# Kernel tuning notes

Hardware: AMD Instinct MI355X
Metric: run time of the kernel (lower is better)

## Reference

```python
import jax, jax.numpy as jnp
import numpy as np

G_K = 16
BN_EPS = 1e-5


def knn_idx(x, k):
    # x: (B, N, C) -> idx: (B, N, k) indices of k nearest neighbors (incl. self)
    sq = jnp.sum(x * x, axis=-1)                       # (B, N)
    d = sq[:, :, None] + sq[:, None, :] - 2.0 * jnp.einsum('bnc,bmc->bnm', x, x)
    _, idx = jax.lax.top_k(-d, k)                      # smallest distances
    return idx


def setup_inputs() -> dict:
    key = jax.random.key(0)
    k1, k2 = jax.random.split(key)
    B, N, C, D = 4, 8192, 3, 64
    x = jax.random.normal(k1, (B, N, C), dtype=jnp.float32)
    W = jax.random.normal(k2, (3 * C, D), dtype=jnp.float32) * 0.1
    b = jnp.zeros((D,), dtype=jnp.float32)
    gamma = jnp.ones((D,), dtype=jnp.float32)
    beta = jnp.zeros((D,), dtype=jnp.float32)
    return {"x": x, "W": W, "b": b, "gamma": gamma, "beta": beta}


def reference(x, W, b, gamma, beta):
    # KNN query (int indices, non-differentiable as in torch)
    idx = knn_idx(x, G_K)                              # (B, N, k)
    # gather-group neighbors: (B, N, k, C)
    x_ne = jax.vmap(lambda xb, ib: xb[ib])(x, idx)
    x_ce = jnp.broadcast_to(x[:, :, None, :], x_ne.shape)
    feat = jnp.concatenate([x_ce, x_ne - x_ce, x_ne], axis=-1)  # (B, N, k, 3C)
    # 1x1 conv == per-(point,neighbor) linear
    h = jnp.einsum('bnkc,cd->bnkd', feat, W) + b       # (B, N, k, D)
    # BatchNorm over (B, N, k) per channel (training-mode batch stats)
    mean = jnp.mean(h, axis=(0, 1, 2))
    var = jnp.var(h, axis=(0, 1, 2))
    h = gamma * (h - mean) * jax.lax.rsqrt(var + BN_EPS) + beta
    h = jax.nn.relu(h)
    # max-pool over neighbors k
    return jnp.max(h, axis=2)                          # (B, N, D)
```

## Files before the change

### kernel.cpp

```cpp
#include <hip/hip_runtime.h>

#define NPTS 8192
#define NB 4
#define KNN 16
#define DCH 64
#define CAP 128
#define WR 8

#define WS_XQ 0
#define WS_XS 524288
#define WS_IB 1048576
#define WS_ST 2097152
#define WS_SS 2097664

__device__ __forceinline__ float vkey(float4 q, float4 c) {
    return __fmaf_rn(q.x, c.x, __fmaf_rn(q.y, c.y, __fmaf_rn(q.z, c.z, c.w)));
}

__global__ __launch_bounds__(256) void k1_prep(const float* __restrict__ x, float4* __restrict__ xq,
                                               float4* __restrict__ xs) {
    int p = blockIdx.x * 256 + threadIdx.x;
    if (p >= NB * NPTS) return;
    float x0 = x[p * 3 + 0], x1 = x[p * 3 + 1], x2 = x[p * 3 + 2];
    float sq = __fmaf_rn(x0, x0, __fmaf_rn(x1, x1, x2 * x2));
    xq[p] = make_float4(x0, x1, x2, sq);
    xs[p] = make_float4(-2.0f * x0, -2.0f * x1, -2.0f * x2, sq);
}

__global__ __launch_bounds__(256, 4) void k2_knn(const float4* __restrict__ xq,
                                                 const float4* __restrict__ xs,
                                                 unsigned short* __restrict__ ibuf) {
    __shared__ float2 buf[4][WR][CAP];
    __shared__ float vmin[4][WR][64];
    const int wave = threadIdx.x >> 6;
    const int lane = threadIdx.x & 63;
    const int b = blockIdx.x >> 8;
    const int blkrow = (blockIdx.x & 255) * (4 * WR);
    const float4* xb = xq + b * NPTS;
    const float4* xc = xs + b * NPTS;
    const int rowbase = blkrow + wave * WR;

    float4 xi[WR];
#pragma unroll
    for (int r = 0; r < WR; ++r) xi[r] = xb[rowbase + r];

    float mn[WR];
#pragma unroll
    for (int r = 0; r < WR; ++r) mn[r] = 3.0e38f;

    {
        const float4* p = xc + lane;
        float4 a0 = p[0], a1 = p[64], a2 = p[128], a3 = p[192];
        for (int c0 = 0; c0 < NPTS - 256; c0 += 256) {
            const float4* pn = p + 256;
            float4 b0 = pn[0], b1 = pn[64], b2 = pn[128], b3 = pn[192];
#pragma unroll
            for (int r = 0; r < WR; ++r) {
                float v0 = vkey(xi[r], a0);
                float v1 = vkey(xi[r], a1);
                float v2 = vkey(xi[r], a2);
                float v3 = vkey(xi[r], a3);
                mn[r] = fminf(mn[r], fminf(v0, v1));
                mn[r] = fminf(mn[r], fminf(v2, v3));
            }
            a0 = b0; a1 = b1; a2 = b2; a3 = b3; p = pn;
        }
#pragma unroll
        for (int r = 0; r < WR; ++r) {
            float v0 = vkey(xi[r], a0);
            float v1 = vkey(xi[r], a1);
            float v2 = vkey(xi[r], a2);
            float v3 = vkey(xi[r], a3);
            mn[r] = fminf(mn[r], fminf(v0, v1));
            mn[r] = fminf(mn[r], fminf(v2, v3));
        }
    }

#pragma unroll
    for (int r = 0; r < WR; ++r) vmin[wave][r][lane] = mn[r];
    __syncthreads();

    float tau[WR];
#pragma unroll
    for (int r = 0; r < WR; ++r) {
        float mine = mn[r];
        int rk = 0;
        const float4* vm4 = (const float4*)(&vmin[wave][r][0]);
#pragma unroll
        for (int q = 0; q < 16; ++q) {
            float4 vv = vm4[q];
            int j0 = q * 4;
            rk += (vv.x < mine || (vv.x == mine && (j0 + 0) < lane)) ? 1 : 0;
            rk += (vv.y < mine || (vv.y == mine && (j0 + 1) < lane)) ? 1 : 0;
            rk += (vv.z < mine || (vv.z == mine && (j0 + 2) < lane)) ? 1 : 0;
            rk += (vv.w < mine || (vv.w == mine && (j0 + 3) < lane)) ? 1 : 0;
        }
        float v = (rk < KNN) ? mine : -3.0e38f;
#pragma unroll
        for (int o = 32; o > 0; o >>= 1) v = fmaxf(v, __shfl_xor(v, o));
        tau[r] = v;
    }

    int cnt[WR];
#pragma unroll
    for (int r = 0; r < WR; ++r) cnt[r] = 0;

    {
        const float4* p = xc + lane;
        float4 a0 = p[0], a1 = p[64], a2 = p[128], a3 = p[192];
        float fl = (float)lane;
        for (int c0 = 0; c0 < NPTS; c0 += 256) {
            bool last = (c0 >= NPTS - 256);
            float4 b0, b1, b2, b3;
            if (!last) {
                const float4* pn = p + 256;
                b0 = pn[0]; b1 = pn[64]; b2 = pn[128]; b3 = pn[192];
            }
            float f0 = (float)c0 + fl;
#pragma unroll
            for (int r = 0; r < WR; ++r) {
                float v0 = vkey(xi[r], a0);
                float v1 = vkey(xi[r], a1);
                float v2 = vkey(xi[r], a2);
                float v3 = vkey(xi[r], a3);
#pragma unroll
                for (int s = 0; s < 4; ++s) {
                    float v = (s == 0) ? v0 : (s == 1) ? v1 : (s == 2) ? v2 : v3;
                    bool pp = (v <= tau[r]);
                    unsigned long long m = __ballot(pp);
                    if (m) {
                        if (pp) {
                            int ofs = __builtin_amdgcn_mbcnt_hi((unsigned)(m >> 32),
                                      __builtin_amdgcn_mbcnt_lo((unsigned)m, 0));
                            int pos = cnt[r] + ofs;
                            if (pos < CAP) buf[wave][r][pos] = make_float2(v, f0 + (float)(s * 64));
                        }
                        cnt[r] += (int)__popcll(m);
                    }
                }
            }
            if (!last) { a0 = b0; a1 = b1; a2 = b2; a3 = b3; p += 256; }
        }
    }

    __syncthreads();

#pragma unroll
    for (int rr = 0; rr < WR; ++rr) {
        int n = cnt[rr];
        n = (n < CAP) ? n : CAP;
        int l1 = lane + 64;
        bool v0 = (lane < n), v1 = (l1 < n);
        float2 e0 = buf[wave][rr][v0 ? lane : 0];
        float2 e1 = buf[wave][rr][v1 ? l1 : 0];
        int r0 = 0, r1 = 0;
        for (int j = 0; j < n; ++j) {
            float2 fj = buf[wave][rr][j];
            r0 += (fj.x < e0.x || (fj.x == e0.x && fj.y < e0.y)) ? 1 : 0;
            r1 += (fj.x < e1.x || (fj.x == e1.x && fj.y < e1.y)) ? 1 : 0;
        }
        size_t grow = (size_t)(b * NPTS + rowbase + rr) * KNN;
        if (v0 && r0 < KNN) ibuf[grow + r0] = (unsigned short)(int)e0.y;
        if (v1 && r1 < KNN) ibuf[grow + r1] = (unsigned short)(int)e1.y;
    }
}

__global__ __launch_bounds__(256) void k3_moments(const float4* __restrict__ xq,
                                                  const unsigned short* __restrict__ ibuf,
                                                  double* __restrict__ stats) {
    __shared__ float red[4][54];
    int p = blockIdx.x * 256 + threadIdx.x;
    int b = p >> 13;
    const float4* xb = xq + b * NPTS;
    const unsigned short* ib = ibuf + (size_t)p * KNN;
    float4 xi = xb[p & (NPTS - 1)];

    float acc[54];
#pragma unroll
    for (int i = 0; i < 54; ++i) acc[i] = 0.0f;

#pragma unroll
    for (int k = 0; k < KNN; ++k) {
        int j = ib[k];
        float4 cj = xb[j];
        float f[9] = {xi.x, xi.y, xi.z, cj.x - xi.x, cj.y - xi.y, cj.z - xi.z, cj.x, cj.y, cj.z};
        int t = 9;
#pragma unroll
        for (int a = 0; a < 9; ++a) {
            acc[a] += f[a];
#pragma unroll
            for (int c = a; c < 9; ++c) { acc[t] += f[a] * f[c]; ++t; }
        }
    }

#pragma unroll
    for (int i = 0; i < 54; ++i) {
        float v = acc[i];
        for (int o = 32; o > 0; o >>= 1) v += __shfl_down(v, o);
        acc[i] = v;
    }
    int lane = threadIdx.x & 63;
    int wv = threadIdx.x >> 6;
    if (lane == 0) {
#pragma unroll
        for (int i = 0; i < 54; ++i) red[wv][i] = acc[i];
    }
    __syncthreads();
    if (threadIdx.x < 54) {
        float s = red[0][threadIdx.x] + red[1][threadIdx.x] + red[2][threadIdx.x] + red[3][threadIdx.x];
        atomicAdd(&stats[threadIdx.x], (double)s);
    }
}

__global__ void k4_finalize(const double* __restrict__ stats, const float* __restrict__ W,
                            const float* __restrict__ bias, const float* __restrict__ gamma,
                            const float* __restrict__ beta, float* __restrict__ ss) {
    int d = threadIdx.x;
    if (d >= DCH) return;
    const double M = (double)NB * NPTS * KNN;
    double w[9];
    for (int c = 0; c < 9; ++c) w[c] = (double)W[c * DCH + d];
    double mf[9];
    for (int a = 0; a < 9; ++a) mf[a] = stats[a] / M;
    double q1 = 0.0;
    for (int a = 0; a < 9; ++a) q1 += mf[a] * w[a];
    double q2 = 0.0;
    int t = 0;
    for (int a = 0; a < 9; ++a) {
        for (int c = a; c < 9; ++c) {
            double pv = stats[9 + t] / M;
            double term = pv * w[a] * w[c];
            q2 += (a == c) ? term : 2.0 * term;
            ++t;
        }
    }
    double bd = (double)bias[d];
    double mean = q1 + bd;
    double ehh = q2 + 2.0 * bd * q1 + bd * bd;
    double var = ehh - mean * mean;
    double sc = (double)gamma[d] / sqrt(var + 1e-5);
    double sh = (double)beta[d] + sc * (bd - mean);
    ss[d] = (float)sc;
    ss[DCH + d] = (float)sh;
}

__global__ __launch_bounds__(256) void k5_out(const float4* __restrict__ xq,
                                              const unsigned short* __restrict__ ibuf,
                                              const float* __restrict__ W, const float* __restrict__ ss,
                                              float* __restrict__ out) {
    __shared__ float Ws[9 * DCH];
    __shared__ float scs[DCH], shs[DCH];
    for (int i = threadIdx.x; i < 9 * DCH; i += 256) Ws[i] = W[i];
    if (threadIdx.x < DCH) {
        scs[threadIdx.x] = ss[threadIdx.x];
        shs[threadIdx.x] = ss[DCH + threadIdx.x];
    }
    __syncthreads();

    int pt = blockIdx.x * 32 + (threadIdx.x >> 3);
    int oc = (threadIdx.x & 7) * 8;
    int b = pt >> 13;
    const float4* xb = xq + b * NPTS;
    float4 xi = xb[pt & (NPTS - 1)];

    float w[9][8];
#pragma unroll
    for (int c = 0; c < 9; ++c)
#pragma unroll
        for (int d = 0; d < 8; ++d) w[c][d] = Ws[c * DCH + oc + d];
    float sc[8], sh[8], y[8];
#pragma unroll
    for (int d = 0; d < 8; ++d) {
        sc[d] = scs[oc + d];
        sh[d] = shs[oc + d];
        y[d] = 0.0f;
    }

    const unsigned short* ib = ibuf + (size_t)pt * KNN;
#pragma unroll
    for (int k = 0; k < KNN; ++k) {
        int j = ib[k];
        float4 cj = xb[j];
        float f[9] = {xi.x, xi.y, xi.z, cj.x - xi.x, cj.y - xi.y, cj.z - xi.z, cj.x, cj.y, cj.z};
        float h[8];
#pragma unroll
        for (int d = 0; d < 8; ++d) h[d] = 0.0f;
#pragma unroll
        for (int c = 0; c < 9; ++c)
#pragma unroll
            for (int d = 0; d < 8; ++d) h[d] = __fmaf_rn(f[c], w[c][d], h[d]);
#pragma unroll
        for (int d = 0; d < 8; ++d) {
            float v = __fmaf_rn(sc[d], h[d], sh[d]);
            y[d] = fmaxf(y[d], fmaxf(v, 0.0f));
        }
    }
    float4* o4 = (float4*)(out + (size_t)pt * DCH + oc);
    o4[0] = make_float4(y[0], y[1], y[2], y[3]);
    o4[1] = make_float4(y[4], y[5], y[6], y[7]);
}

extern "C" void kernel_launch(void* const* d_in, const int* in_sizes, int n_in,
                              void* d_out, int out_size, void* d_ws, size_t ws_size,
                              hipStream_t stream) {
    const float* x = (const float*)d_in[0];
    const float* W = (const float*)d_in[1];
    const float* bias = (const float*)d_in[2];
    const float* gamma = (const float*)d_in[3];
    const float* beta = (const float*)d_in[4];
    float* out = (float*)d_out;
    char* ws = (char*)d_ws;

    float4* xq = (float4*)(ws + WS_XQ);
    float4* xs = (float4*)(ws + WS_XS);
    unsigned short* ibuf = (unsigned short*)(ws + WS_IB);
    double* stats = (double*)(ws + WS_ST);
    float* ss = (float*)(ws + WS_SS);

    hipMemsetAsync(stats, 0, 54 * sizeof(double), stream);
    k1_prep<<<128, 256, 0, stream>>>(x, xq, xs);
    k2_knn<<<1024, 256, 0, stream>>>(xq, xs, ibuf);
    k3_moments<<<128, 256, 0, stream>>>(xq, ibuf, stats);
    k4_finalize<<<1, 64, 0, stream>>>(stats, W, bias, gamma, beta, ss);
    k5_out<<<1024, 256, 0, stream>>>(xq, ibuf, W, ss, out);
}
```

Before: 136.5 us.

## Use packed FP32 FMA in KNN scan with SoA-of-4 candidate layout

Candidate points are stored in blocks of four as separate x, y, z and squared-norm float4 vectors, so each lane loads four consecutive candidates. The distance keys are then computed with two-wide vector FMAs, which can map to packed FP32 instructions on CDNA and halve the FMA issue count. Candidate index encoding changes from strided (s*64) to consecutive (s), and the running minimum is split into two accumulators. The costs are extra register pressure from the broadcast query vectors and a different global access pattern per lane.

```diff
diff --git a/kernel.cpp b/kernel.cpp
--- a/kernel.cpp
+++ b/kernel.cpp
@@ -7,24 +7,34 @@
 #define CAP 128
 #define WR 8
 
+typedef float f32x2 __attribute__((ext_vector_type(2)));
+
 #define WS_XQ 0
 #define WS_XS 524288
 #define WS_IB 1048576
 #define WS_ST 2097152
 #define WS_SS 2097664
 
-__device__ __forceinline__ float vkey(float4 q, float4 c) {
-    return __fmaf_rn(q.x, c.x, __fmaf_rn(q.y, c.y, __fmaf_rn(q.z, c.z, c.w)));
+__device__ __forceinline__ f32x2 vkey2(f32x2 qx, f32x2 qy, f32x2 qz,
+                                       f32x2 cx, f32x2 cy, f32x2 cz, f32x2 cw) {
+    return __builtin_elementwise_fma(qx, cx,
+           __builtin_elementwise_fma(qy, cy,
+           __builtin_elementwise_fma(qz, cz, cw)));
 }
 
 __global__ __launch_bounds__(256) void k1_prep(const float* __restrict__ x, float4* __restrict__ xq,
-                                               float4* __restrict__ xs) {
+                                               float* __restrict__ xsb) {
     int p = blockIdx.x * 256 + threadIdx.x;
     if (p >= NB * NPTS) return;
     float x0 = x[p * 3 + 0], x1 = x[p * 3 + 1], x2 = x[p * 3 + 2];
     float sq = __fmaf_rn(x0, x0, __fmaf_rn(x1, x1, x2 * x2));
     xq[p] = make_float4(x0, x1, x2, sq);
-    xs[p] = make_float4(-2.0f * x0, -2.0f * x1, -2.0f * x2, sq);
+    int k = p >> 2, s = p & 3;
+    size_t base = (size_t)k * 16 + s;
+    xsb[base + 0]  = -2.0f * x0;
+    xsb[base + 4]  = -2.0f * x1;
+    xsb[base + 8]  = -2.0f * x2;
+    xsb[base + 12] = sq;
 }
 
 __global__ __launch_bounds__(256, 4) void k2_knn(const float4* __restrict__ xq,
@@ -37,44 +47,59 @@
     const int b = blockIdx.x >> 8;
     const int blkrow = (blockIdx.x & 255) * (4 * WR);
     const float4* xb = xq + b * NPTS;
-    const float4* xc = xs + b * NPTS;
+    const float4* xc = xs + (size_t)b * NPTS;
     const int rowbase = blkrow + wave * WR;
 
-    float4 xi[WR];
-#pragma unroll
-    for (int r = 0; r < WR; ++r) xi[r] = xb[rowbase + r];
-
-    float mn[WR];
-#pragma unroll
-    for (int r = 0; r < WR; ++r) mn[r] = 3.0e38f;
+    f32x2 qx2[WR], qy2[WR], qz2[WR];
+#pragma unroll
+    for (int r = 0; r < WR; ++r) {
+        float4 xi = xb[rowbase + r];
+        qx2[r] = (f32x2){xi.x, xi.x};
+        qy2[r] = (f32x2){xi.y, xi.y};
+        qz2[r] = (f32x2){xi.z, xi.z};
+    }
+
+    float mna[WR], mnb[WR];
+#pragma unroll
+    for (int r = 0; r < WR; ++r) { mna[r] = 3.0e38f; mnb[r] = 3.0e38f; }
 
     {
-        const float4* p = xc + lane;
-        float4 a0 = p[0], a1 = p[64], a2 = p[128], a3 = p[192];
+        const float4* p = xc + lane * 4;
+        float4 X = p[0], Y = p[1], Z = p[2], W = p[3];
         for (int c0 = 0; c0 < NPTS - 256; c0 += 256) {
             const float4* pn = p + 256;
-            float4 b0 = pn[0], b1 = pn[64], b2 = pn[128], b3 = pn[192];
+            float4 Xn = pn[0], Yn = pn[1], Zn = pn[2], Wn = pn[3];
+            f32x2 Xa = {X.x, X.y}, Xb = {X.z, X.w};
+            f32x2 Ya = {Y.x, Y.y}, Yb = {Y.z, Y.w};
+            f32x2 Za = {Z.x, Z.y}, Zb = {Z.z, Z.w};
+            f32x2 Wa = {W.x, W.y}, Wb = {W.z, W.w};
 #pragma unroll
             for (int r = 0; r < WR; ++r) {
-                float v0 = vkey(xi[r], a0);
-                float v1 = vkey(xi[r], a1);
-                float v2 = vkey(xi[r], a2);
-                float v3 = vkey(xi[r], a3);
-                mn[r] = fminf(mn[r], fminf(v0, v1));
-                mn[r] = fminf(mn[r], fminf(v2, v3));
+                f32x2 va = vkey2(qx2[r], qy2[r], qz2[r], Xa, Ya, Za, Wa);
+                f32x2 vb = vkey2(qx2[r], qy2[r], qz2[r], Xb, Yb, Zb, Wb);
+                mna[r] = fminf(mna[r], fminf(va.x, vb.x));
+                mnb[r] = fminf(mnb[r], fminf(va.y, vb.y));
             }
-            a0 = b0; a1 = b1; a2 = b2; a3 = b3; p = pn;
-        }
-#pragma unroll
-        for (int r = 0; r < WR; ++r) {
-            float v0 = vkey(xi[r], a0);
-            float v1 = vkey(xi[r], a1);
-            float v2 = vkey(xi[r], a2);
-            float v3 = vkey(xi[r], a3);
-            mn[r] = fminf(mn[r], fminf(v0, v1));
-            mn[r] = fminf(mn[r], fminf(v2, v3));
-        }
-    }
+            X = Xn; Y = Yn; Z = Zn; W = Wn; p = pn;
+        }
+        {
+            f32x2 Xa = {X.x, X.y}, Xb = {X.z, X.w};
+            f32x2 Ya = {Y.x, Y.y}, Yb = {Y.z, Y.w};
+            f32x2 Za = {Z.x, Z.y}, Zb = {Z.z, Z.w};
+            f32x2 Wa = {W.x, W.y}, Wb = {W.z, W.w};
+#pragma unroll
+            for (int r = 0; r < WR; ++r) {
+                f32x2 va = vkey2(qx2[r], qy2[r], qz2[r], Xa, Ya, Za, Wa);
+                f32x2 vb = vkey2(qx2[r], qy2[r], qz2[r], Xb, Yb, Zb, Wb);
+                mna[r] = fminf(mna[r], fminf(va.x, vb.x));
+                mnb[r] = fminf(mnb[r], fminf(va.y, vb.y));
+            }
+        }
+    }
+
+    float mn[WR];
+#pragma unroll
+    for (int r = 0; r < WR; ++r) mn[r] = fminf(mna[r], mnb[r]);
 
 #pragma unroll
     for (int r = 0; r < WR; ++r) vmin[wave][r][lane] = mn[r];
@@ -106,26 +131,29 @@
     for (int r = 0; r < WR; ++r) cnt[r] = 0;
 
     {
-        const float4* p = xc + lane;
-        float4 a0 = p[0], a1 = p[64], a2 = p[128], a3 = p[192];
-        float fl = (float)lane;
+        const float4* p = xc + lane * 4;
+        float4 X = p[0], Y = p[1], Z = p[2], W = p[3];
+        float fl4 = (float)(lane << 2);
         for (int c0 = 0; c0 < NPTS; c0 += 256) {
             bool last = (c0 >= NPTS - 256);
-            float4 b0, b1, b2, b3;
+            float4 Xn, Yn, Zn, Wn;
             if (!last) {
                 const float4* pn = p + 256;
-                b0 = pn[0]; b1 = pn[64]; b2 = pn[128]; b3 = pn[192];
+                Xn = pn[0]; Yn = pn[1]; Zn = pn[2]; Wn = pn[3];
             }
-            float f0 = (float)c0 + fl;
+            f32x2 Xa = {X.x, X.y}, Xb = {X.z, X.w};
+            f32x2 Ya = {Y.x, Y.y}, Yb = {Y.z, Y.w};
+            f32x2 Za = {Z.x, Z.y}, Zb = {Z.z, Z.w};
+            f32x2 Wa = {W.x, W.y}, Wb = {W.z, W.w};
+            float f0 = (float)c0 + fl4;
 #pragma unroll
             for (int r = 0; r < WR; ++r) {
-                float v0 = vkey(xi[r], a0);
-                float v1 = vkey(xi[r], a1);
-                float v2 = vkey(xi[r], a2);
-                float v3 = vkey(xi[r], a3);
+                f32x2 va = vkey2(qx2[r], qy2[r], qz2[r], Xa, Ya, Za, Wa);
+                f32x2 vb = vkey2(qx2[r], qy2[r], qz2[r], Xb, Yb, Zb, Wb);
+                float vs[4] = {va.x, va.y, vb.x, vb.y};
 #pragma unroll
                 for (int s = 0; s < 4; ++s) {
-                    float v = (s == 0) ? v0 : (s == 1) ? v1 : (s == 2) ? v2 : v3;
+                    float v = vs[s];
                     bool pp = (v <= tau[r]);
                     unsigned long long m = __ballot(pp);
                     if (m) {
@@ -133,13 +161,13 @@
                             int ofs = __builtin_amdgcn_mbcnt_hi((unsigned)(m >> 32),
                                       __builtin_amdgcn_mbcnt_lo((unsigned)m, 0));
                             int pos = cnt[r] + ofs;
-                            if (pos < CAP) buf[wave][r][pos] = make_float2(v, f0 + (float)(s * 64));
+                            if (pos < CAP) buf[wave][r][pos] = make_float2(v, f0 + (float)s);
                         }
                         cnt[r] += (int)__popcll(m);
                     }
                 }
             }
-            if (!last) { a0 = b0; a1 = b1; a2 = b2; a3 = b3; p += 256; }
+            if (!last) { X = Xn; Y = Yn; Z = Zn; W = Wn; p += 256; }
         }
     }
 
@@ -318,7 +346,7 @@
     float* ss = (float*)(ws + WS_SS);
 
     hipMemsetAsync(stats, 0, 54 * sizeof(double), stream);
-    k1_prep<<<128, 256, 0, stream>>>(x, xq, xs);
+    k1_prep<<<128, 256, 0, stream>>>(x, xq, (float*)xs);
     k2_knn<<<1024, 256, 0, stream>>>(xq, xs, ibuf);
     k3_moments<<<128, 256, 0, stream>>>(xq, ibuf, stats);
     k4_finalize<<<1, 64, 0, stream>>>(stats, W, bias, gamma, beta, ss);
```

Measured after the change: 149.7 us. 1.1x slower.
